# Optimization experiments

Hardware: AMD Instinct MI355X
Metric: run time of the kernel (lower is better)

The kernel has to match this reference:

```python
import jax, jax.numpy as jnp
import numpy as np

CHUNK = 400
L = 50          # encoder kernel and stride
JUMP = CHUNK // L  # 8 new frames per streaming step
N = 128         # encoder feature dim
B = 128         # bottleneck dim
H = 512         # TCN hidden dim
K = 3           # depthwise kernel size
R, X = 2, 7     # repeats x blocks, dilations 2^0..2^6
BUF = 516       # ring buffer length: JUMP + 2*sum(dilations)*R = 8 + 508
EPS = 1e-8


def setup_inputs() -> dict:
    key = jax.random.key(0)
    ks = jax.random.split(key, 16)
    nb = R * X
    w = lambda i, shape: jax.random.normal(ks[i], shape, jnp.float32) * 0.05
    return dict(
        mixture=jax.random.normal(ks[0], (1, 2, CHUNK), jnp.float32),
        encoder_buffer=jax.random.uniform(ks[1], (1, N, BUF), dtype=jnp.float32),
        layernorm_buffer=jax.random.normal(ks[2], (1, B, BUF), jnp.float32),
        W_enc=w(3, (N, 2, L)),              # encoder Conv1d(2->N, k=L, s=L)
        ln_g=jnp.ones((N,), jnp.float32),    # channelwise LayerNorm affine
        ln_b=jnp.zeros((N,), jnp.float32),
        W_bn=w(4, (B, N)),                   # bottleneck 1x1 conv
        blk_w1=w(5, (nb, H, B)),             # per-block pointwise in
        blk_p1=jnp.full((nb,), 0.25, jnp.float32),
        blk_g1=jnp.ones((nb, H), jnp.float32),
        blk_b1=jnp.zeros((nb, H), jnp.float32),
        blk_dw=w(6, (nb, H, K)),             # depthwise dilated conv
        blk_p2=jnp.full((nb,), 0.25, jnp.float32),
        blk_g2=jnp.ones((nb, H), jnp.float32),
        blk_b2=jnp.zeros((nb, H), jnp.float32),
        blk_w2=w(7, (nb, B, H)),             # per-block pointwise out
        W_mask=w(8, (N, B)),                 # mask 1x1 conv (C=1 source)
        W_dec=w(9, (L, N)),                  # decoder basis Linear(N->L)
    )


def _cln(x, g, b):
    # channelwise LayerNorm: normalize over channel dim per time frame. x: [1,C,T]
    mu = jnp.mean(x, axis=1, keepdims=True)
    var = jnp.var(x, axis=1, keepdims=True)
    return g[None, :, None] * (x - mu) * jax.lax.rsqrt(var + EPS) + b[None, :, None]


def _prelu(x, a):
    return jnp.where(x >= 0, x, a * x)


def _dwconv(x, w, d):
    # valid dilated depthwise conv. x: [1,H,T], w: [H,K] -> [1,H,T-(K-1)*d]
    return jax.lax.conv_general_dilated(
        x, w[:, None, :], window_strides=(1,), padding='VALID',
        rhs_dilation=(d,), feature_group_count=H,
        dimension_numbers=('NCH', 'OIH', 'NCH'))


def reference(mixture, encoder_buffer, layernorm_buffer, W_enc, ln_g, ln_b, W_bn,
              blk_w1, blk_p1, blk_g1, blk_b1, blk_dw, blk_p2, blk_g2, blk_b2,
              blk_w2, W_mask, W_dec):
    # --- encoder: Conv1d(2->N, k=L, s=L) + ReLU -> JUMP new frames, ring-shift buffer
    enc = jax.nn.relu(jax.lax.conv_general_dilated(
        mixture, W_enc, window_strides=(L,), padding='VALID',
        dimension_numbers=('NCH', 'OIH', 'NCH')))          # [1,N,JUMP]
    encoder_buffer = jnp.concatenate([encoder_buffer[:, :, JUMP:], enc], axis=2)

    # --- separator front-end (network[0:2]): cLN + bottleneck 1x1, per-frame causal
    ln_new = jnp.einsum('oc,bct->bot', W_bn, _cln(enc, ln_g, ln_b))  # [1,B,JUMP]
    layernorm_buffer = jnp.concatenate([layernorm_buffer[:, :, JUMP:], ln_new], axis=2)

    # --- TCN (network[2]): valid causal dilated blocks, each shrinks time by 2*d
    x = layernorm_buffer                                   # [1,B,516]
    for i in range(R * X):
        d = 2 ** (i % X)
        y = jnp.einsum('hc,bct->bht', blk_w1[i], x)
        y = _cln(_prelu(y, blk_p1[i]), blk_g1[i], blk_b1[i])
        y = _dwconv(y, blk_dw[i], d)                       # time -= (K-1)*d
        y = _cln(_prelu(y, blk_p2[i]), blk_g2[i], blk_b2[i])
        y = jnp.einsum('ch,bht->bct', blk_w2[i], y)
        x = x[:, :, (K - 1) * d:] + y                      # residual on trailing frames
    # x: [1,B,JUMP]

    # --- mask conv (network[3]) + ReLU, reshape to [1,C=1,N,JUMP]
    mask = jax.nn.relu(jnp.einsum('nc,bct->bnt', W_mask, x)).reshape(1, 1, N, JUMP)

    # --- decoder: mask the newest JUMP encoder frames, basis Linear(N->L), stride=L
    src_w = encoder_buffer[:, None, :, -JUMP:] * mask      # [1,1,N,JUMP]
    est_source = jnp.einsum('ln,bcnt->bctl', W_dec, src_w).reshape(1, 1, JUMP * L)
    return est_source, encoder_buffer, layernorm_buffer
```

## Files before the change

### kernel.cpp

```cpp
#include <hip/hip_runtime.h>

#define CHUNK 400
#define LWIN 50
#define JUMP 8
#define NCH 128
#define BCH 128
#define HCH 512
#define NBLK 14
#define BUF 516
#define SHIFT 508
#define EPSV 1e-8f
#define NWG 136

__device__ __forceinline__ void cstore(float* p, float v) {
    __hip_atomic_store(p, v, __ATOMIC_RELAXED, __HIP_MEMORY_SCOPE_AGENT);
}
__device__ __forceinline__ float cload(const float* p) {
    return __hip_atomic_load(p, __ATOMIC_RELAXED, __HIP_MEMORY_SCOPE_AGENT);
}

__device__ __forceinline__ void fwait(unsigned* flp, int base, int cnt, int tid) {
    if (tid < cnt) {
        unsigned* p = flp + base + tid;
        while (__hip_atomic_load(p, __ATOMIC_RELAXED, __HIP_MEMORY_SCOPE_AGENT) == 0)
            __builtin_amdgcn_s_sleep(1);
    }
    __syncthreads();
}
__device__ __forceinline__ void fset(unsigned* flp, int idx, int tid) {
    __syncthreads();
    if (tid == 0)
        __hip_atomic_store(flp + idx, 1u, __ATOMIC_RELAXED, __HIP_MEMORY_SCOPE_AGENT);
}

__device__ __forceinline__ void stage1_core(
    int tid, int lane, int wid, int t0, int nf,
    const float* __restrict__ w1b, float aPr,
    const float* __restrict__ gv, const float* __restrict__ bv,
    float* __restrict__ yout, float* redf, float* statsf, const float* xsv)
{
    float acc[4] = {0.f, 0.f, 0.f, 0.f};
    const float4* __restrict__ wr = (const float4*)(w1b + (size_t)tid * BCH);
    const float4* __restrict__ xv = (const float4*)xsv;
    #pragma unroll 4
    for (int c4 = 0; c4 < 32; ++c4) {
        float4 w = wr[c4];
        #pragma unroll
        for (int f = 0; f < 4; ++f) {
            float4 x = xv[f * 32 + c4];
            acc[f] += w.x * x.x + w.y * x.y + w.z * x.z + w.w * x.w;
        }
    }
    #pragma unroll
    for (int f = 0; f < 4; ++f) acc[f] = acc[f] >= 0.f ? acc[f] : aPr * acc[f];
    for (int f = 0; f < nf; ++f) {
        float s = acc[f], q = acc[f] * acc[f];
        #pragma unroll
        for (int o = 32; o; o >>= 1) { s += __shfl_xor(s, o); q += __shfl_xor(q, o); }
        if (lane == 0) { redf[(wid * 4 + f) * 2] = s; redf[(wid * 4 + f) * 2 + 1] = q; }
    }
    __syncthreads();
    if (tid < nf) {
        float s = 0.f, q = 0.f;
        #pragma unroll
        for (int w = 0; w < 8; ++w) { s += redf[(w * 4 + tid) * 2]; q += redf[(w * 4 + tid) * 2 + 1]; }
        float mean = s * (1.f / HCH);
        float var = q * (1.f / HCH) - mean * mean;
        statsf[tid * 2] = mean; statsf[tid * 2 + 1] = rsqrtf(var + EPSV);
    }
    __syncthreads();
    float gg = gv[tid], bb = bv[tid];
    for (int f = 0; f < nf; ++f)
        cstore(&yout[(t0 + f) * HCH + tid],
               gg * (acc[f] - statsf[f * 2]) * statsf[f * 2 + 1] + bb);
}

__global__ __launch_bounds__(512) void k_fused(
    const float* __restrict__ mixture, const float* __restrict__ inEnc,
    const float* __restrict__ inLn, const float* __restrict__ Wenc,
    const float* __restrict__ lng, const float* __restrict__ lnb,
    const float* __restrict__ Wbn, const float* __restrict__ w1,
    const float* __restrict__ p1, const float* __restrict__ g1,
    const float* __restrict__ b1, const float* __restrict__ dwc,
    const float* __restrict__ p2, const float* __restrict__ g2,
    const float* __restrict__ b2, const float* __restrict__ w2,
    const float* __restrict__ Wmask, const float* __restrict__ Wdec,
    float* __restrict__ est, float* __restrict__ outEnc, float* __restrict__ outLn,
    unsigned* __restrict__ fl, float* __restrict__ enc,
    float* __restrict__ xbuf, float* __restrict__ ybuf)
{
    __shared__ float xs[4 * BCH];
    __shared__ float ys[4 * 528];
    __shared__ float redf[8 * 4 * 2];
    __shared__ float statsf[4 * 2];

    const int wg = blockIdx.x;
    const int tid = threadIdx.x;
    const int lane = tid & 63, wid = tid >> 6;
    const int j = wg;
    const size_t xstr = (size_t)BUF * BCH;
    const size_t ystr = (size_t)BUF * HCH;

    if (wg < 8) {
        int t = wg;
        float e = 0.f;
        if (tid < 128) {
            int c = tid;
            const float* w = Wenc + c * 100;
            const float* m = mixture + t * LWIN;
            #pragma unroll 10
            for (int l = 0; l < LWIN; ++l) e += m[l] * w[l] + m[CHUNK + l] * w[LWIN + l];
            e = fmaxf(e, 0.f);
            cstore(&enc[t * NCH + c], e);
            outEnc[c * BUF + SHIFT + t] = e;
            float s = e, q = e * e;
            #pragma unroll
            for (int o = 32; o; o >>= 1) { s += __shfl_xor(s, o); q += __shfl_xor(q, o); }
            if (lane == 0) { redf[(wid * 4) * 2] = s; redf[(wid * 4) * 2 + 1] = q; }
        }
        __syncthreads();
        if (tid < 128) {
            float S = redf[0] + redf[8], Q = redf[1] + redf[9];
            float mean = S * (1.f / NCH);
            float var = Q * (1.f / NCH) - mean * mean;
            float r = rsqrtf(var + EPSV);
            xs[tid] = lng[tid] * (e - mean) * r + lnb[tid];
        }
        __syncthreads();
        if (tid < 128) {
            float acc = 0.f;
            const float4* wr = (const float4*)(Wbn + tid * NCH);
            const float4* nv = (const float4*)xs;
            #pragma unroll 8
            for (int j4 = 0; j4 < 32; ++j4) {
                float4 w = wr[j4]; float4 x = nv[j4];
                acc += w.x * x.x + w.y * x.y + w.z * x.z + w.w * x.w;
            }
            outLn[tid * BUF + SHIFT + t] = acc;
            cstore(&xbuf[(SHIFT + t) * BCH + tid], acc);
        }
    } else {
        int ch = wg - 8;
        for (int t = tid; t < SHIFT; t += 512)
            outEnc[ch * BUF + t] = inEnc[ch * BUF + t + JUMP];
        if (ch < 127) {
            int f = tid >> 7, c = tid & 127;
            int t = 4 * ch + f;
            float v = inLn[c * BUF + t + JUMP];
            cstore(&xbuf[t * BCH + c], v);
            outLn[c * BUF + t] = v;
        }
    }
    fset(fl, 0 * NWG + wg, tid);

    if (4 * j < BUF) {
        int base, cnt;
        if (j <= 126)      { base = 8 + j; cnt = 1; }
        else if (j == 127) { base = 0;     cnt = 4; }
        else               { base = 4;     cnt = 4; }
        fwait(fl, base, cnt, tid);
        int t0 = 4 * j;
        int nf = min(4, BUF - t0);
        for (int idx = tid; idx < nf * BCH; idx += 512) xs[idx] = cload(&xbuf[t0 * BCH + idx]);
        __syncthreads();
        stage1_core(tid, lane, wid, t0, nf, w1, p1[0], g1, b1, ybuf, redf, statsf, xs);
    }
    fset(fl, 1 * NWG + wg, tid);

    int T = BUF;
    for (int i = 0; i < NBLK; ++i) {
        const float* xin = xbuf + (size_t)(i & 1) * xstr;
        float* xout      = xbuf + (size_t)((i + 1) & 1) * xstr;
        const float* ycur = ybuf + (size_t)(i & 1) * ystr;
        float* ynext      = ybuf + (size_t)((i + 1) & 1) * ystr;
        int d = 1 << (i % 7);
        int Tout = T - 2 * d;
        int t0 = 4 * j;
        if (t0 < Tout) {
            int jmaxe = (T - 1) >> 2;
            int jmax = min(j + ((3 + 2 * d) >> 2), jmaxe);
            int woff = (i >= 1 && i < NBLK - 1) ? ((3 + 2 * (1 << ((i - 1) % 7))) >> 2) : 0;
            int jlo = max(0, j - woff);
            fwait(fl + (1 + i) * NWG, jlo, jmax - jlo + 1, tid);
            if (i == NBLK - 1) fwait(fl, 4 * j, 4, tid);
            int nf = min(4, Tout - t0);
            const float* dwb = dwc + (size_t)i * HCH * 3;
            float d0 = dwb[tid * 3], d1 = dwb[tid * 3 + 1], d2 = dwb[tid * 3 + 2];
            float a2 = p2[i];
            float y[4];
            for (int f = 0; f < nf; ++f) {
                int t = t0 + f;
                float v = d0 * cload(&ycur[t * HCH + tid])
                        + d1 * cload(&ycur[(t + d) * HCH + tid])
                        + d2 * cload(&ycur[(t + 2 * d) * HCH + tid]);
                y[f] = v >= 0.f ? v : a2 * v;
            }
            for (int f = 0; f < nf; ++f) {
                float s = y[f], q = y[f] * y[f];
                #pragma unroll
                for (int o = 32; o; o >>= 1) { s += __shfl_xor(s, o); q += __shfl_xor(q, o); }
                if (lane == 0) { redf[(wid * 4 + f) * 2] = s; redf[(wid * 4 + f) * 2 + 1] = q; }
            }
            __syncthreads();
            if (tid < nf) {
                float s = 0.f, q = 0.f;
                #pragma unroll
                for (int w = 0; w < 8; ++w) { s += redf[(w * 4 + tid) * 2]; q += redf[(w * 4 + tid) * 2 + 1]; }
                float mean = s * (1.f / HCH);
                float var = q * (1.f / HCH) - mean * mean;
                statsf[tid * 2] = mean; statsf[tid * 2 + 1] = rsqrtf(var + EPSV);
            }
            __syncthreads();
            {
                float gg = g2[i * HCH + tid], bb = b2[i * HCH + tid];
                int pidx = (tid >> 7) * 132 + (tid & 127);
                for (int f = 0; f < nf; ++f)
                    ys[f * 528 + pidx] = gg * (y[f] - statsf[f * 2]) * statsf[f * 2 + 1] + bb;
            }
            __syncthreads();
            int c = tid >> 2, p = tid & 3;
            float acc[4] = {0.f, 0.f, 0.f, 0.f};
            const float4* wr = (const float4*)(w2 + (size_t)i * BCH * HCH + c * HCH + p * 128);
            const float* yb = ys + p * 132;
            #pragma unroll 4
            for (int j4 = 0; j4 < 32; ++j4) {
                float4 w = wr[j4];
                #pragma unroll
                for (int f = 0; f < 4; ++f) {
                    float4 x = *(const float4*)&yb[f * 528 + j4 * 4];
                    acc[f] += w.x * x.x + w.y * x.y + w.z * x.z + w.w * x.w;
                }
            }
            for (int f = 0; f < nf; ++f) {
                acc[f] += __shfl_xor(acc[f], 1);
                acc[f] += __shfl_xor(acc[f], 2);
            }
            if (p == 0) {
                for (int f = 0; f < nf; ++f) {
                    int t = t0 + f;
                    float xv = cload(&xin[(t + 2 * d) * BCH + c]) + acc[f];
                    cstore(&xout[t * BCH + c], xv);
                    xs[f * BCH + c] = xv;
                }
            }
            __syncthreads();
            if (i < NBLK - 1) {
                stage1_core(tid, lane, wid, t0, nf,
                            w1 + (size_t)(i + 1) * HCH * BCH, p1[i + 1],
                            g1 + (i + 1) * HCH, b1 + (i + 1) * HCH, ynext, redf, statsf, xs);
            } else {
                int cc = tid & 127, f = tid >> 7;
                float m = 0.f;
                const float4* wm = (const float4*)(Wmask + cc * BCH);
                const float4* xv = (const float4*)(xs + f * BCH);
                #pragma unroll 8
                for (int j4 = 0; j4 < 32; ++j4) {
                    float4 w = wm[j4]; float4 x = xv[j4];
                    m += w.x * x.x + w.y * x.y + w.z * x.z + w.w * x.w;
                }
                m = fmaxf(m, 0.f);
                ys[f * BCH + cc] = m * cload(&enc[(t0 + f) * NCH + cc]);
                __syncthreads();
                if (tid < 4 * LWIN) {
                    int ff = tid / LWIN, l = tid % LWIN;
                    float e = 0.f;
                    const float4* wd = (const float4*)(Wdec + l * NCH);
                    const float4* sv = (const float4*)(ys + ff * BCH);
                    #pragma unroll 8
                    for (int j4 = 0; j4 < 32; ++j4) {
                        float4 w = wd[j4]; float4 x = sv[j4];
                        e += w.x * x.x + w.y * x.y + w.z * x.z + w.w * x.w;
                    }
                    est[(t0 + ff) * LWIN + l] = e;
                }
            }
        }
        fset(fl, (2 + i) * NWG + wg, tid);
        T = Tout;
    }
}

extern "C" void kernel_launch(void* const* d_in, const int* in_sizes, int n_in,
                              void* d_out, int out_size, void* d_ws, size_t ws_size,
                              hipStream_t stream) {
    const float* mixture = (const float*)d_in[0];
    const float* inEnc   = (const float*)d_in[1];
    const float* inLn    = (const float*)d_in[2];
    const float* Wenc    = (const float*)d_in[3];
    const float* lng     = (const float*)d_in[4];
    const float* lnb     = (const float*)d_in[5];
    const float* Wbn     = (const float*)d_in[6];
    const float* w1      = (const float*)d_in[7];
    const float* p1      = (const float*)d_in[8];
    const float* g1      = (const float*)d_in[9];
    const float* b1      = (const float*)d_in[10];
    const float* dwc     = (const float*)d_in[11];
    const float* p2      = (const float*)d_in[12];
    const float* g2      = (const float*)d_in[13];
    const float* b2      = (const float*)d_in[14];
    const float* w2      = (const float*)d_in[15];
    const float* Wmask   = (const float*)d_in[16];
    const float* Wdec    = (const float*)d_in[17];

    float* est    = (float*)d_out;
    float* outEnc = est + CHUNK;
    float* outLn  = outEnc + NCH * BUF;

    unsigned* fl = (unsigned*)d_ws;
    float* enc  = (float*)d_ws + 2304;
    float* xbuf = enc + 1024;
    float* ybuf = xbuf + 2 * (size_t)BUF * BCH;

    hipMemsetAsync(d_ws, 0, 9216, stream);

    void* args[] = { &mixture, &inEnc, &inLn, &Wenc, &lng, &lnb, &Wbn, &w1, &p1,
                     &g1, &b1, &dwc, &p2, &g2, &b2, &w2, &Wmask, &Wdec,
                     &est, &outEnc, &outLn, &fl, &enc, &xbuf, &ybuf };
    hipLaunchCooperativeKernel((const void*)k_fused, dim3(NWG), dim3(512),
                               (void**)args, 0, stream);
}
```

Baseline: 379.5 us.

## Vectorize coherent cross-workgroup loads and stores with dwordx4 cache-bypass asm

Replaces the scalar relaxed atomic loads and stores on the shared ring buffers (xbuf, ybuf) with 128-bit global loads and stores marked sc0 sc1 in inline asm, staging values through LDS so each access is contiguous and vectorized. The depthwise conv stage is remapped so each thread handles 4 channels of one frame instead of 1 channel over 4 frames, and the reductions and norm are adjusted to match. The aim is to cut the number of slow system-coherent memory transactions on the latency-bound streaming path. The cost is extra LDS staging and __syncthreads barriers, and the inline asm waits on vmcnt(0) after every load, which serializes it.

```diff
diff --git a/kernel.cpp b/kernel.cpp
--- a/kernel.cpp
+++ b/kernel.cpp
@@ -12,6 +12,32 @@
 #define EPSV 1e-8f
 #define NWG 136
 
+typedef float f4v __attribute__((ext_vector_type(4)));
+
+__device__ __forceinline__ void cstore4(float* p, float4 v) {
+    f4v t = {v.x, v.y, v.z, v.w};
+    asm volatile("global_store_dwordx4 %0, %1, off sc0 sc1"
+                 :: "v"(p), "v"(t) : "memory");
+}
+__device__ __forceinline__ float4 cload4(const float* p) {
+    f4v t;
+    asm volatile("global_load_dwordx4 %0, %1, off sc0 sc1\n\ts_waitcnt vmcnt(0)"
+                 : "=v"(t) : "v"(p) : "memory");
+    return make_float4(t.x, t.y, t.z, t.w);
+}
+__device__ __forceinline__ void cload4x3(float4& a, float4& b, float4& c,
+        const float* pa, const float* pb, const float* pc) {
+    f4v ta, tb, tc;
+    asm volatile("global_load_dwordx4 %0, %3, off sc0 sc1\n\t"
+                 "global_load_dwordx4 %1, %4, off sc0 sc1\n\t"
+                 "global_load_dwordx4 %2, %5, off sc0 sc1\n\t"
+                 "s_waitcnt vmcnt(0)"
+                 : "=&v"(ta), "=&v"(tb), "=&v"(tc)
+                 : "v"(pa), "v"(pb), "v"(pc) : "memory");
+    a = make_float4(ta.x, ta.y, ta.z, ta.w);
+    b = make_float4(tb.x, tb.y, tb.z, tb.w);
+    c = make_float4(tc.x, tc.y, tc.z, tc.w);
+}
 __device__ __forceinline__ void cstore(float* p, float v) {
     __hip_atomic_store(p, v, __ATOMIC_RELAXED, __HIP_MEMORY_SCOPE_AGENT);
 }
@@ -37,7 +63,8 @@
     int tid, int lane, int wid, int t0, int nf,
     const float* __restrict__ w1b, float aPr,
     const float* __restrict__ gv, const float* __restrict__ bv,
-    float* __restrict__ yout, float* redf, float* statsf, const float* xsv)
+    float* __restrict__ yout, float* redf, float* statsf,
+    const float* xsv, float* ysT)
 {
     float acc[4] = {0.f, 0.f, 0.f, 0.f};
     const float4* __restrict__ wr = (const float4*)(w1b + (size_t)tid * BCH);
@@ -71,8 +98,11 @@
     __syncthreads();
     float gg = gv[tid], bb = bv[tid];
     for (int f = 0; f < nf; ++f)
-        cstore(&yout[(t0 + f) * HCH + tid],
-               gg * (acc[f] - statsf[f * 2]) * statsf[f * 2 + 1] + bb);
+        ysT[f * HCH + tid] = gg * (acc[f] - statsf[f * 2]) * statsf[f * 2 + 1] + bb;
+    __syncthreads();
+    int f2 = tid >> 7, h4 = tid & 127;
+    if (f2 < nf)
+        cstore4(&yout[(t0 + f2) * HCH + 4 * h4], *(float4*)&ysT[f2 * HCH + 4 * h4]);
 }
 
 __global__ __launch_bounds__(512) void k_fused(
@@ -137,8 +167,11 @@
                 acc += w.x * x.x + w.y * x.y + w.z * x.z + w.w * x.w;
             }
             outLn[tid * BUF + SHIFT + t] = acc;
-            cstore(&xbuf[(SHIFT + t) * BCH + tid], acc);
-        }
+            ys[tid] = acc;
+        }
+        __syncthreads();
+        if (tid < 32)
+            cstore4(&xbuf[(SHIFT + t) * BCH + 4 * tid], *(float4*)&ys[4 * tid]);
     } else {
         int ch = wg - 8;
         for (int t = tid; t < SHIFT; t += 512)
@@ -147,8 +180,13 @@
             int f = tid >> 7, c = tid & 127;
             int t = 4 * ch + f;
             float v = inLn[c * BUF + t + JUMP];
-            cstore(&xbuf[t * BCH + c], v);
             outLn[c * BUF + t] = v;
+            ys[f * BCH + c] = v;
+        }
+        __syncthreads();
+        if (ch < 127 && tid < 128) {
+            int f = tid >> 5, c4 = tid & 31;
+            cstore4(&xbuf[(4 * ch + f) * BCH + 4 * c4], *(float4*)&ys[f * BCH + 4 * c4]);
         }
     }
     fset(fl, 0 * NWG + wg, tid);
@@ -161,9 +199,12 @@
         fwait(fl, base, cnt, tid);
         int t0 = 4 * j;
         int nf = min(4, BUF - t0);
-        for (int idx = tid; idx < nf * BCH; idx += 512) xs[idx] = cload(&xbuf[t0 * BCH + idx]);
-        __syncthreads();
-        stage1_core(tid, lane, wid, t0, nf, w1, p1[0], g1, b1, ybuf, redf, statsf, xs);
+        if (tid < nf * 32) {
+            float4 v = cload4(&xbuf[t0 * BCH + 4 * tid]);
+            *(float4*)&xs[4 * tid] = v;
+        }
+        __syncthreads();
+        stage1_core(tid, lane, wid, t0, nf, w1, p1[0], g1, b1, ybuf, redf, statsf, xs, ys);
     }
     fset(fl, 1 * NWG + wg, tid);
 
@@ -184,38 +225,54 @@
             fwait(fl + (1 + i) * NWG, jlo, jmax - jlo + 1, tid);
             if (i == NBLK - 1) fwait(fl, 4 * j, 4, tid);
             int nf = min(4, Tout - t0);
-            const float* dwb = dwc + (size_t)i * HCH * 3;
-            float d0 = dwb[tid * 3], d1 = dwb[tid * 3 + 1], d2 = dwb[tid * 3 + 2];
-            float a2 = p2[i];
-            float y[4];
-            for (int f = 0; f < nf; ++f) {
-                int t = t0 + f;
-                float v = d0 * cload(&ycur[t * HCH + tid])
-                        + d1 * cload(&ycur[(t + d) * HCH + tid])
-                        + d2 * cload(&ycur[(t + 2 * d) * HCH + tid]);
-                y[f] = v >= 0.f ? v : a2 * v;
-            }
-            for (int f = 0; f < nf; ++f) {
-                float s = y[f], q = y[f] * y[f];
+            const int f = tid >> 7, h4 = tid & 127;
+            float4 yv; yv.x = yv.y = yv.z = yv.w = 0.f;
+            if (f < nf) {
+                float4 ya, yb2, yc;
+                cload4x3(ya, yb2, yc,
+                         &ycur[(t0 + f) * HCH + 4 * h4],
+                         &ycur[(t0 + f + d) * HCH + 4 * h4],
+                         &ycur[(t0 + f + 2 * d) * HCH + 4 * h4]);
+                const float* dwb = dwc + (size_t)i * HCH * 3 + 12 * h4;
+                float4 w0 = *(const float4*)(dwb);
+                float4 w1v = *(const float4*)(dwb + 4);
+                float4 w2v = *(const float4*)(dwb + 8);
+                float a2 = p2[i];
+                yv.x = w0.x * ya.x + w0.y * yb2.x + w0.z * yc.x;
+                yv.y = w0.w * ya.y + w1v.x * yb2.y + w1v.y * yc.y;
+                yv.z = w1v.z * ya.z + w1v.w * yb2.z + w2v.x * yc.z;
+                yv.w = w2v.y * ya.w + w2v.z * yb2.w + w2v.w * yc.w;
+                yv.x = yv.x >= 0.f ? yv.x : a2 * yv.x;
+                yv.y = yv.y >= 0.f ? yv.y : a2 * yv.y;
+                yv.z = yv.z >= 0.f ? yv.z : a2 * yv.z;
+                yv.w = yv.w >= 0.f ? yv.w : a2 * yv.w;
+            }
+            {
+                float s = yv.x + yv.y + yv.z + yv.w;
+                float q = yv.x * yv.x + yv.y * yv.y + yv.z * yv.z + yv.w * yv.w;
                 #pragma unroll
                 for (int o = 32; o; o >>= 1) { s += __shfl_xor(s, o); q += __shfl_xor(q, o); }
-                if (lane == 0) { redf[(wid * 4 + f) * 2] = s; redf[(wid * 4 + f) * 2 + 1] = q; }
+                if (lane == 0 && f < nf) { redf[wid * 2] = s; redf[wid * 2 + 1] = q; }
             }
             __syncthreads();
             if (tid < nf) {
-                float s = 0.f, q = 0.f;
-                #pragma unroll
-                for (int w = 0; w < 8; ++w) { s += redf[(w * 4 + tid) * 2]; q += redf[(w * 4 + tid) * 2 + 1]; }
+                float s = redf[4 * tid] + redf[4 * tid + 2];
+                float q = redf[4 * tid + 1] + redf[4 * tid + 3];
                 float mean = s * (1.f / HCH);
                 float var = q * (1.f / HCH) - mean * mean;
                 statsf[tid * 2] = mean; statsf[tid * 2 + 1] = rsqrtf(var + EPSV);
             }
             __syncthreads();
-            {
-                float gg = g2[i * HCH + tid], bb = b2[i * HCH + tid];
-                int pidx = (tid >> 7) * 132 + (tid & 127);
-                for (int f = 0; f < nf; ++f)
-                    ys[f * 528 + pidx] = gg * (y[f] - statsf[f * 2]) * statsf[f * 2 + 1] + bb;
+            if (f < nf) {
+                float mean = statsf[f * 2], rstd = statsf[f * 2 + 1];
+                float4 gv = *(const float4*)&g2[i * HCH + 4 * h4];
+                float4 bv = *(const float4*)&b2[i * HCH + 4 * h4];
+                float4 nv;
+                nv.x = gv.x * (yv.x - mean) * rstd + bv.x;
+                nv.y = gv.y * (yv.y - mean) * rstd + bv.y;
+                nv.z = gv.z * (yv.z - mean) * rstd + bv.z;
+                nv.w = gv.w * (yv.w - mean) * rstd + bv.w;
+                *(float4*)&ys[f * 528 + (h4 >> 5) * 132 + (h4 & 31) * 4] = nv;
             }
             __syncthreads();
             int c = tid >> 2, p = tid & 3;
@@ -226,40 +283,46 @@
             for (int j4 = 0; j4 < 32; ++j4) {
                 float4 w = wr[j4];
                 #pragma unroll
-                for (int f = 0; f < 4; ++f) {
-                    float4 x = *(const float4*)&yb[f * 528 + j4 * 4];
-                    acc[f] += w.x * x.x + w.y * x.y + w.z * x.z + w.w * x.w;
+                for (int ff = 0; ff < 4; ++ff) {
+                    float4 x = *(const float4*)&yb[ff * 528 + j4 * 4];
+                    acc[ff] += w.x * x.x + w.y * x.y + w.z * x.z + w.w * x.w;
                 }
             }
-            for (int f = 0; f < nf; ++f) {
-                acc[f] += __shfl_xor(acc[f], 1);
-                acc[f] += __shfl_xor(acc[f], 2);
-            }
-            if (p == 0) {
-                for (int f = 0; f < nf; ++f) {
-                    int t = t0 + f;
-                    float xv = cload(&xin[(t + 2 * d) * BCH + c]) + acc[f];
-                    cstore(&xout[t * BCH + c], xv);
-                    xs[f * BCH + c] = xv;
+            for (int ff = 0; ff < nf; ++ff) {
+                acc[ff] += __shfl_xor(acc[ff], 1);
+                acc[ff] += __shfl_xor(acc[ff], 2);
+            }
+            if (p == 0)
+                for (int ff = 0; ff < nf; ++ff) xs[ff * BCH + c] = acc[ff];
+            __syncthreads();
+            if (tid < 128) {
+                int f2 = tid >> 5, c4 = tid & 31;
+                if (f2 < nf) {
+                    float4 xr = cload4(&xin[(t0 + f2 + 2 * d) * BCH + 4 * c4]);
+                    float4 xa = *(float4*)&xs[f2 * BCH + 4 * c4];
+                    xa.x += xr.x; xa.y += xr.y; xa.z += xr.z; xa.w += xr.w;
+                    *(float4*)&xs[f2 * BCH + 4 * c4] = xa;
+                    cstore4(&xout[(t0 + f2) * BCH + 4 * c4], xa);
                 }
             }
             __syncthreads();
             if (i < NBLK - 1) {
                 stage1_core(tid, lane, wid, t0, nf,
                             w1 + (size_t)(i + 1) * HCH * BCH, p1[i + 1],
-                            g1 + (i + 1) * HCH, b1 + (i + 1) * HCH, ynext, redf, statsf, xs);
+                            g1 + (i + 1) * HCH, b1 + (i + 1) * HCH, ynext,
+                            redf, statsf, xs, ys);
             } else {
-                int cc = tid & 127, f = tid >> 7;
+                int cc = tid & 127, f3 = tid >> 7;
                 float m = 0.f;
                 const float4* wm = (const float4*)(Wmask + cc * BCH);
-                const float4* xv = (const float4*)(xs + f * BCH);
+                const float4* xv = (const float4*)(xs + f3 * BCH);
                 #pragma unroll 8
                 for (int j4 = 0; j4 < 32; ++j4) {
                     float4 w = wm[j4]; float4 x = xv[j4];
                     m += w.x * x.x + w.y * x.y + w.z * x.z + w.w * x.w;
                 }
                 m = fmaxf(m, 0.f);
-                ys[f * BCH + cc] = m * cload(&enc[(t0 + f) * NCH + cc]);
+                ys[f3 * BCH + cc] = m * cload(&enc[(t0 + f3) * NCH + cc]);
                 __syncthreads();
                 if (tid < 4 * LWIN) {
                     int ff = tid / LWIN, l = tid % LWIN;
@@ -311,11 +374,11 @@
     float* xbuf = enc + 1024;
     float* ybuf = xbuf + 2 * (size_t)BUF * BCH;
 
-    hipMemsetAsync(d_ws, 0, 9216, stream);
+    (void)hipMemsetAsync(d_ws, 0, 9216, stream);
 
     void* args[] = { &mixture, &inEnc, &inLn, &Wenc, &lng, &lnb, &Wbn, &w1, &p1,
                      &g1, &b1, &dwc, &p2, &g2, &b2, &w2, &Wmask, &Wdec,
                      &est, &outEnc, &outLn, &fl, &enc, &xbuf, &ybuf };
-    hipLaunchCooperativeKernel((const void*)k_fused, dim3(NWG), dim3(512),
-                               (void**)args, 0, stream);
-}
+    (void)hipLaunchCooperativeKernel((const void*)k_fused, dim3(NWG), dim3(512),
+                                     (void**)args, 0, stream);
+}
```

Result: faster. 332.4 us (-12.4%).
